# Kernel optimization log

Measured on AMD Instinct MI355X. Metric: run time of the kernel, lower is better.

The kernel has to match this reference:

```python
import jax, jax.numpy as jnp
import numpy as np

NUM_NODES = 100000
NUM_EDGES = 400000
EPS = 1e-9


def _find(parent, u):
    # chase parent pointers to the root (no path compression; parent is
    # immutable within one find, so this terminates because union-by-rank
    # keeps the forest acyclic)
    return jax.lax.while_loop(lambda v: parent[v] != v, lambda v: parent[v], u)


def _kruskal(scores, edge_index, num_nodes):
    """Greedy Kruskal over edges sorted by descending score, via union-find.
    Returns b in {0,1}^E with exactly (num_nodes-1) ones if the graph is
    connected (fewer otherwise), identical acceptance set to the torch loop."""
    E = scores.shape[0]
    order = jnp.argsort(-scores)  # descending
    src = edge_index[0].astype(jnp.int32)
    dst = edge_index[1].astype(jnp.int32)
    max_used = jnp.int32(num_nodes - 1)

    def step(carry, idx):
        parent, rank, b, used = carry
        i = src[idx]
        j = dst[idx]
        ru = _find(parent, i)
        rv = _find(parent, j)
        accept = (ru != rv) & (used < max_used)
        ri = rank[ru]
        rj = rank[rv]
        # union by rank: if ri<rj attach ru under rv, else attach rv under ru;
        # if ranks equal, root ru gains rank (matches the torch union())
        child = jnp.where(ri < rj, ru, rv)
        root = jnp.where(ri < rj, rv, ru)
        parent = parent.at[child].set(jnp.where(accept, root, parent[child]))
        rank = rank.at[root].add(jnp.where(accept & (ri == rj), jnp.int32(1), jnp.int32(0)))
        b = b.at[idx].set(accept.astype(b.dtype))
        used = used + accept.astype(used.dtype)
        return (parent, rank, b, used), None

    parent0 = jnp.arange(num_nodes, dtype=jnp.int32)
    rank0 = jnp.zeros(num_nodes, dtype=jnp.int32)
    b0 = jnp.zeros(E, dtype=scores.dtype)
    (parent, rank, b, used), _ = jax.lax.scan(step, (parent0, rank0, b0, jnp.int32(0)), order)
    return b


def setup_inputs() -> dict:
    key = jax.random.key(0)
    k1, k2, k3 = jax.random.split(key, 3)
    s = jax.random.normal(k1, (NUM_EDGES,), dtype=jnp.float32)
    u = jax.random.uniform(k2, (NUM_EDGES,), dtype=jnp.float32)
    edge_index = jax.random.randint(k3, (2, NUM_EDGES), 0, NUM_NODES, dtype=jnp.int32)
    return {"s": s, "u": u, "edge_index": edge_index, "num_nodes": NUM_NODES}


def reference(s, u, edge_index, num_nodes):
    s_prob = jax.nn.sigmoid(s)
    gumbel = -jnp.log(-jnp.log(u + EPS) + EPS)
    scores = s_prob + gumbel
    return _kruskal(scores, edge_index, num_nodes)
```

## Files before the change

### kernel.cpp

```cpp
#include <hip/hip_runtime.h>
#include <stdint.h>

#define V_NODES 100000
#define MAX_ROUNDS 13
#define TB 256
#define RPT 4
#define TBL 2048
#define TBL_FROM 3

struct alignas(16) Rec { unsigned long long k; unsigned int a, b; };

__device__ __forceinline__ unsigned long long make_key(float sv, float uv, int id) {
    float sp = 1.0f / (1.0f + expf(-sv));
    float g  = -logf(-logf(uv + 1e-9f) + 1e-9f);
    unsigned int b = __float_as_uint(sp + g);
    unsigned int m = (b & 0x80000000u) ? ~b : (b | 0x80000000u);
    return ((unsigned long long)(~m) << 19) | (unsigned long long)(unsigned)id;
}

__device__ __forceinline__ int find_root(const int* __restrict__ parent, int v) {
    int p = parent[v];
    int pp = parent[p];
    while (p != pp) { p = pp; pp = parent[p]; }
    return p;
}

__device__ __forceinline__ void gbid(unsigned long long* __restrict__ best,
                                     unsigned int* __restrict__ guess,
                                     unsigned int root, unsigned long long k) {
    unsigned int kh = (unsigned int)(k >> 32);
    unsigned int g = guess[root];
    if (kh > g) return;
    if (kh < g) guess[root] = kh;
    atomicMin(&best[root], k);
}

__global__ void k_scan0(const float* __restrict__ s, const float* __restrict__ u,
                        const int* __restrict__ src, const int* __restrict__ dst,
                        float* __restrict__ out, unsigned long long* __restrict__ best,
                        unsigned int* __restrict__ guess,
                        Rec* __restrict__ recs, int* __restrict__ parent,
                        int* __restrict__ flags, int E) {
    int base = (blockIdx.x * TB + threadIdx.x) * RPT;

    float sv[RPT], uv[RPT];
    unsigned int a[RPT], b[RPT];
    #pragma unroll
    for (int j = 0; j < RPT; ++j) {
        int e = base + j;
        if (e < E) { sv[j] = s[e]; uv[j] = u[e]; a[j] = src[e]; b[j] = dst[e]; }
    }

    Rec r[RPT];
    #pragma unroll
    for (int j = 0; j < RPT; ++j) {
        int e = base + j;
        if (e >= E) continue;
        r[j].k = make_key(sv[j], uv[j], e);
        r[j].a = a[j]; r[j].b = b[j];
        recs[e] = r[j];
        out[e] = 0.0f;
        if (e < V_NODES) parent[e] = e;
        if (e < MAX_ROUNDS) flags[e] = (e == 0) ? 1 : 0;
    }

    #pragma unroll
    for (int j = 0; j < RPT; ++j) {
        int e = base + j;
        if (e >= E || a[j] == b[j]) continue;
        gbid(best, guess, a[j], r[j].k);
        gbid(best, guess, b[j], r[j].k);
    }
}

__global__ void k_scan_early(const int* __restrict__ parent,
                             unsigned long long* __restrict__ bestC,
                             unsigned int* __restrict__ guess,
                             Rec* __restrict__ recs, int* __restrict__ flags,
                             int r, int E) {
    __shared__ int sflag;
    if (flags[r - 1] == 0) return;
    if (threadIdx.x == 0) sflag = 0;
    __syncthreads();

    int base = (blockIdx.x * TB + threadIdx.x) * RPT;
    bool cross = false;

    Rec rec[RPT];
    int pa[RPT], pb[RPT];
    bool live[RPT];
    #pragma unroll
    for (int j = 0; j < RPT; ++j) {
        int i = base + j;
        if (i < E) rec[j] = recs[i];
        else { rec[j].a = 0; rec[j].b = 0; }
        live[j] = (rec[j].a != rec[j].b);
    }
    #pragma unroll
    for (int j = 0; j < RPT; ++j)
        if (live[j]) { pa[j] = parent[rec[j].a]; pb[j] = parent[rec[j].b]; }

    #pragma unroll
    for (int j = 0; j < RPT; ++j) {
        if (!live[j]) continue;
        int i = base + j;
        int ra = pa[j], rb = pb[j];
        int p = parent[ra]; while (ra != p) { ra = p; p = parent[ra]; }
        p = parent[rb];     while (rb != p) { rb = p; p = parent[rb]; }
        if (ra == rb) {
            *(uint2*)&recs[i].a = make_uint2((unsigned)ra, (unsigned)ra);
        } else {
            cross = true;
            if ((unsigned)ra != rec[j].a || (unsigned)rb != rec[j].b)
                *(uint2*)&recs[i].a = make_uint2((unsigned)ra, (unsigned)rb);
            gbid(bestC, guess, (unsigned)ra, rec[j].k);
            gbid(bestC, guess, (unsigned)rb, rec[j].k);
        }
    }
    if (cross) sflag = 1;
    __syncthreads();
    if (threadIdx.x == 0 && sflag) flags[r] = 1;
}

__global__ void k_scan_tbl(const int* __restrict__ parent,
                           unsigned long long* __restrict__ bestC,
                           unsigned int* __restrict__ guess,
                           Rec* __restrict__ recs, int* __restrict__ flags,
                           int r, int E) {
    __shared__ int sflag;
    __shared__ unsigned int tag[TBL];
    __shared__ unsigned long long tkey[TBL];
    if (flags[r - 1] == 0) return;
    for (int t = threadIdx.x; t < TBL; t += TB) { tag[t] = 0xFFFFFFFFu; tkey[t] = ~0ULL; }
    if (threadIdx.x == 0) sflag = 0;
    __syncthreads();

    int base = (blockIdx.x * TB + threadIdx.x) * RPT;
    bool cross = false;

    Rec rec[RPT];
    int pa[RPT], pb[RPT];
    bool live[RPT];
    #pragma unroll
    for (int j = 0; j < RPT; ++j) {
        int i = base + j;
        if (i < E) rec[j] = recs[i];
        else { rec[j].a = 0; rec[j].b = 0; }
        live[j] = (rec[j].a != rec[j].b);
    }
    #pragma unroll
    for (int j = 0; j < RPT; ++j)
        if (live[j]) { pa[j] = parent[rec[j].a]; pb[j] = parent[rec[j].b]; }
    #pragma unroll
    for (int j = 0; j < RPT; ++j)
        if (live[j]) { pa[j] = parent[pa[j]]; pb[j] = parent[pb[j]]; }

    auto bid = [&](unsigned int root, unsigned long long k) {
        unsigned int s1 = root & (TBL - 1);
        unsigned int prev = atomicCAS(&tag[s1], 0xFFFFFFFFu, root);
        if (prev == 0xFFFFFFFFu || prev == root) {
            atomicMin(&tkey[s1], k);
            return;
        }
        unsigned int s2 = (root * 2654435761u >> 19) & (TBL - 1);
        prev = atomicCAS(&tag[s2], 0xFFFFFFFFu, root);
        if (prev == 0xFFFFFFFFu || prev == root) {
            atomicMin(&tkey[s2], k);
            return;
        }
        gbid(bestC, guess, root, k);
    };

    #pragma unroll
    for (int j = 0; j < RPT; ++j) {
        if (!live[j]) continue;
        int i = base + j;
        int ra = pa[j], rb = pb[j];
        int p = parent[ra]; while (ra != p) { ra = p; p = parent[ra]; }
        p = parent[rb];     while (rb != p) { rb = p; p = parent[rb]; }
        if (ra == rb) {
            *(uint2*)&recs[i].a = make_uint2((unsigned)ra, (unsigned)ra);
        } else {
            cross = true;
            if ((unsigned)ra != rec[j].a || (unsigned)rb != rec[j].b)
                *(uint2*)&recs[i].a = make_uint2((unsigned)ra, (unsigned)rb);
            bid((unsigned)ra, rec[j].k);
            bid((unsigned)rb, rec[j].k);
        }
    }
    if (cross) sflag = 1;
    __syncthreads();

    for (int t = threadIdx.x; t < TBL; t += TB) {
        unsigned int rt = tag[t];
        if (rt != 0xFFFFFFFFu) gbid(bestC, guess, rt, tkey[t]);
    }
    if (threadIdx.x == 0 && sflag) flags[r] = 1;
}

__global__ void k_choose(const int* __restrict__ src, const int* __restrict__ dst,
                         int* __restrict__ parent,
                         const unsigned long long* __restrict__ bestC,
                         float* __restrict__ out, const int* __restrict__ flags,
                         int r) {
    if (flags[r] == 0) return;
    int v = blockIdx.x * blockDim.x + threadIdx.x;
    if (v >= V_NODES) return;
    unsigned long long k = bestC[v];
    if ((unsigned)(k >> 51) != 0u) return;
    int id = (int)(unsigned int)(k & 0x7FFFFu);
    int a0 = src[id], b0 = dst[id];
    int ru = find_root(parent, a0);
    int rv = find_root(parent, b0);
    if (ru != a0) parent[a0] = ru;
    if (rv != b0) parent[b0] = rv;
    int other = (ru == v) ? rv : ru;
    out[id] = 1.0f;
    if ((bestC[other] != k || v > other) && other != v) {
        int po = parent[other];
        parent[v] = (po != other) ? po : other;
    }
}

extern "C" void kernel_launch(void* const* d_in, const int* in_sizes, int n_in,
                              void* d_out, int out_size, void* d_ws, size_t ws_size,
                              hipStream_t stream) {
    const float* s  = (const float*)d_in[0];
    const float* u  = (const float*)d_in[1];
    const int*   ei = (const int*)d_in[2];
    const int E = in_sizes[0];
    const int* src = ei;
    const int* dst = ei + E;
    float* out = (float*)d_out;

    char* ws = (char*)d_ws;
    Rec* recs = (Rec*)ws;
    unsigned long long* bestAll = (unsigned long long*)(recs + E);
    int* parent = (int*)(bestAll + (size_t)MAX_ROUNDS * V_NODES);
    unsigned int* guessAll = (unsigned int*)(parent + V_NODES);
    int* flags  = (int*)(guessAll + (size_t)MAX_ROUNDS * V_NODES);

    const int gE4 = (E + TB * RPT - 1) / (TB * RPT);
    const int gV  = (V_NODES + TB - 1) / TB;

    k_scan0<<<gE4, TB, 0, stream>>>(s, u, src, dst, out, bestAll, guessAll,
                                    recs, parent, flags, E);
    k_choose<<<gV, TB, 0, stream>>>(src, dst, parent, bestAll, out, flags, 0);

    for (int r = 1; r < MAX_ROUNDS; ++r) {
        unsigned long long* best_r = bestAll + (size_t)r * V_NODES;
        unsigned int* guess_r = guessAll + (size_t)r * V_NODES;
        if (r < TBL_FROM)
            k_scan_early<<<gE4, TB, 0, stream>>>(parent, best_r, guess_r,
                                                 recs, flags, r, E);
        else
            k_scan_tbl<<<gE4, TB, 0, stream>>>(parent, best_r, guess_r,
                                               recs, flags, r, E);
        k_choose<<<gV, TB, 0, stream>>>(src, dst, parent, best_r, out, flags, r);
    }
}
```

Measured before the change: 270.3 us.

## Replace parent-array union-find with pointer jumping over previous round's best-edge keys

Removes the per-round k_choose kernel and the parent array. Each scan now finds a component root by following the previous round's min-edge hooks, resolving mutual pairs by the lower id. All chosen edges are marked in one final k_mark pass over every round's best arrays. This cuts 13 launches and the parent writes, but root lookup now chases chains of 64-bit best keys plus record loads, which can be long in later rounds.

```diff
diff --git a/kernel.cpp b/kernel.cpp
--- a/kernel.cpp
+++ b/kernel.cpp
@@ -16,13 +16,6 @@
     unsigned int b = __float_as_uint(sp + g);
     unsigned int m = (b & 0x80000000u) ? ~b : (b | 0x80000000u);
     return ((unsigned long long)(~m) << 19) | (unsigned long long)(unsigned)id;
-}
-
-__device__ __forceinline__ int find_root(const int* __restrict__ parent, int v) {
-    int p = parent[v];
-    int pp = parent[p];
-    while (p != pp) { p = pp; pp = parent[p]; }
-    return p;
 }
 
 __device__ __forceinline__ void gbid(unsigned long long* __restrict__ best,
@@ -35,12 +28,27 @@
     atomicMin(&best[root], k);
 }
 
+__device__ __forceinline__ unsigned int resolve(
+        const unsigned long long* __restrict__ bestP,
+        const Rec* __restrict__ recs,
+        unsigned int x, unsigned long long kb) {
+    while (!(kb >> 51)) {
+        unsigned int id = (unsigned int)(kb & 0x7FFFFu);
+        uint2 ab = *(const uint2*)&recs[id].a;
+        unsigned int other = (ab.x == x) ? ab.y : ab.x;
+        if (other == x) break;
+        unsigned long long ko = bestP[other];
+        if (ko == kb && x < other) break;
+        x = other; kb = ko;
+    }
+    return x;
+}
+
 __global__ void k_scan0(const float* __restrict__ s, const float* __restrict__ u,
                         const int* __restrict__ src, const int* __restrict__ dst,
                         float* __restrict__ out, unsigned long long* __restrict__ best,
                         unsigned int* __restrict__ guess,
-                        Rec* __restrict__ recs, int* __restrict__ parent,
-                        int* __restrict__ flags, int E) {
+                        Rec* __restrict__ recs, int* __restrict__ flags, int E) {
     int base = (blockIdx.x * TB + threadIdx.x) * RPT;
 
     float sv[RPT], uv[RPT];
@@ -60,7 +68,6 @@
         r[j].a = a[j]; r[j].b = b[j];
         recs[e] = r[j];
         out[e] = 0.0f;
-        if (e < V_NODES) parent[e] = e;
         if (e < MAX_ROUNDS) flags[e] = (e == 0) ? 1 : 0;
     }
 
@@ -73,7 +80,7 @@
     }
 }
 
-__global__ void k_scan_early(const int* __restrict__ parent,
+__global__ void k_scan_early(const unsigned long long* __restrict__ bestP,
                              unsigned long long* __restrict__ bestC,
                              unsigned int* __restrict__ guess,
                              Rec* __restrict__ recs, int* __restrict__ flags,
@@ -87,7 +94,7 @@
     bool cross = false;
 
     Rec rec[RPT];
-    int pa[RPT], pb[RPT];
+    unsigned long long ka[RPT], kb[RPT];
     bool live[RPT];
     #pragma unroll
     for (int j = 0; j < RPT; ++j) {
@@ -98,23 +105,22 @@
     }
     #pragma unroll
     for (int j = 0; j < RPT; ++j)
-        if (live[j]) { pa[j] = parent[rec[j].a]; pb[j] = parent[rec[j].b]; }
+        if (live[j]) { ka[j] = bestP[rec[j].a]; kb[j] = bestP[rec[j].b]; }
 
     #pragma unroll
     for (int j = 0; j < RPT; ++j) {
         if (!live[j]) continue;
         int i = base + j;
-        int ra = pa[j], rb = pb[j];
-        int p = parent[ra]; while (ra != p) { ra = p; p = parent[ra]; }
-        p = parent[rb];     while (rb != p) { rb = p; p = parent[rb]; }
+        unsigned int ra = resolve(bestP, recs, rec[j].a, ka[j]);
+        unsigned int rb = resolve(bestP, recs, rec[j].b, kb[j]);
         if (ra == rb) {
-            *(uint2*)&recs[i].a = make_uint2((unsigned)ra, (unsigned)ra);
+            *(uint2*)&recs[i].a = make_uint2(ra, ra);
         } else {
             cross = true;
-            if ((unsigned)ra != rec[j].a || (unsigned)rb != rec[j].b)
-                *(uint2*)&recs[i].a = make_uint2((unsigned)ra, (unsigned)rb);
-            gbid(bestC, guess, (unsigned)ra, rec[j].k);
-            gbid(bestC, guess, (unsigned)rb, rec[j].k);
+            if (ra != rec[j].a || rb != rec[j].b)
+                *(uint2*)&recs[i].a = make_uint2(ra, rb);
+            gbid(bestC, guess, ra, rec[j].k);
+            gbid(bestC, guess, rb, rec[j].k);
         }
     }
     if (cross) sflag = 1;
@@ -122,7 +128,7 @@
     if (threadIdx.x == 0 && sflag) flags[r] = 1;
 }
 
-__global__ void k_scan_tbl(const int* __restrict__ parent,
+__global__ void k_scan_tbl(const unsigned long long* __restrict__ bestP,
                            unsigned long long* __restrict__ bestC,
                            unsigned int* __restrict__ guess,
                            Rec* __restrict__ recs, int* __restrict__ flags,
@@ -139,7 +145,7 @@
     bool cross = false;
 
     Rec rec[RPT];
-    int pa[RPT], pb[RPT];
+    unsigned long long ka[RPT], kb[RPT];
     bool live[RPT];
     #pragma unroll
     for (int j = 0; j < RPT; ++j) {
@@ -150,10 +156,7 @@
     }
     #pragma unroll
     for (int j = 0; j < RPT; ++j)
-        if (live[j]) { pa[j] = parent[rec[j].a]; pb[j] = parent[rec[j].b]; }
-    #pragma unroll
-    for (int j = 0; j < RPT; ++j)
-        if (live[j]) { pa[j] = parent[pa[j]]; pb[j] = parent[pb[j]]; }
+        if (live[j]) { ka[j] = bestP[rec[j].a]; kb[j] = bestP[rec[j].b]; }
 
     auto bid = [&](unsigned int root, unsigned long long k) {
         unsigned int s1 = root & (TBL - 1);
@@ -175,17 +178,16 @@
     for (int j = 0; j < RPT; ++j) {
         if (!live[j]) continue;
         int i = base + j;
-        int ra = pa[j], rb = pb[j];
-        int p = parent[ra]; while (ra != p) { ra = p; p = parent[ra]; }
-        p = parent[rb];     while (rb != p) { rb = p; p = parent[rb]; }
+        unsigned int ra = resolve(bestP, recs, rec[j].a, ka[j]);
+        unsigned int rb = resolve(bestP, recs, rec[j].b, kb[j]);
         if (ra == rb) {
-            *(uint2*)&recs[i].a = make_uint2((unsigned)ra, (unsigned)ra);
+            *(uint2*)&recs[i].a = make_uint2(ra, ra);
         } else {
             cross = true;
-            if ((unsigned)ra != rec[j].a || (unsigned)rb != rec[j].b)
-                *(uint2*)&recs[i].a = make_uint2((unsigned)ra, (unsigned)rb);
-            bid((unsigned)ra, rec[j].k);
-            bid((unsigned)rb, rec[j].k);
+            if (ra != rec[j].a || rb != rec[j].b)
+                *(uint2*)&recs[i].a = make_uint2(ra, rb);
+            bid(ra, rec[j].k);
+            bid(rb, rec[j].k);
         }
     }
     if (cross) sflag = 1;
@@ -198,27 +200,14 @@
     if (threadIdx.x == 0 && sflag) flags[r] = 1;
 }
 
-__global__ void k_choose(const int* __restrict__ src, const int* __restrict__ dst,
-                         int* __restrict__ parent,
-                         const unsigned long long* __restrict__ bestC,
-                         float* __restrict__ out, const int* __restrict__ flags,
-                         int r) {
-    if (flags[r] == 0) return;
-    int v = blockIdx.x * blockDim.x + threadIdx.x;
+__global__ void k_mark(const unsigned long long* __restrict__ bestAll,
+                       float* __restrict__ out) {
+    int v = blockIdx.x * TB + threadIdx.x;
     if (v >= V_NODES) return;
-    unsigned long long k = bestC[v];
-    if ((unsigned)(k >> 51) != 0u) return;
-    int id = (int)(unsigned int)(k & 0x7FFFFu);
-    int a0 = src[id], b0 = dst[id];
-    int ru = find_root(parent, a0);
-    int rv = find_root(parent, b0);
-    if (ru != a0) parent[a0] = ru;
-    if (rv != b0) parent[b0] = rv;
-    int other = (ru == v) ? rv : ru;
-    out[id] = 1.0f;
-    if ((bestC[other] != k || v > other) && other != v) {
-        int po = parent[other];
-        parent[v] = (po != other) ? po : other;
+    #pragma unroll
+    for (int r = 0; r < MAX_ROUNDS; ++r) {
+        unsigned long long k = bestAll[(size_t)r * V_NODES + v];
+        if (!(k >> 51)) out[(unsigned int)(k & 0x7FFFFu)] = 1.0f;
     }
 }
 
@@ -236,26 +225,26 @@
     char* ws = (char*)d_ws;
     Rec* recs = (Rec*)ws;
     unsigned long long* bestAll = (unsigned long long*)(recs + E);
-    int* parent = (int*)(bestAll + (size_t)MAX_ROUNDS * V_NODES);
-    unsigned int* guessAll = (unsigned int*)(parent + V_NODES);
+    unsigned int* guessAll = (unsigned int*)(bestAll + (size_t)MAX_ROUNDS * V_NODES);
     int* flags  = (int*)(guessAll + (size_t)MAX_ROUNDS * V_NODES);
 
     const int gE4 = (E + TB * RPT - 1) / (TB * RPT);
     const int gV  = (V_NODES + TB - 1) / TB;
 
     k_scan0<<<gE4, TB, 0, stream>>>(s, u, src, dst, out, bestAll, guessAll,
-                                    recs, parent, flags, E);
-    k_choose<<<gV, TB, 0, stream>>>(src, dst, parent, bestAll, out, flags, 0);
+                                    recs, flags, E);
 
     for (int r = 1; r < MAX_ROUNDS; ++r) {
+        unsigned long long* best_p = bestAll + (size_t)(r - 1) * V_NODES;
         unsigned long long* best_r = bestAll + (size_t)r * V_NODES;
         unsigned int* guess_r = guessAll + (size_t)r * V_NODES;
         if (r < TBL_FROM)
-            k_scan_early<<<gE4, TB, 0, stream>>>(parent, best_r, guess_r,
+            k_scan_early<<<gE4, TB, 0, stream>>>(best_p, best_r, guess_r,
                                                  recs, flags, r, E);
         else
-            k_scan_tbl<<<gE4, TB, 0, stream>>>(parent, best_r, guess_r,
+            k_scan_tbl<<<gE4, TB, 0, stream>>>(best_p, best_r, guess_r,
                                                recs, flags, r, E);
-        k_choose<<<gV, TB, 0, stream>>>(src, dst, parent, best_r, out, flags, r);
-    }
-}
+    }
+
+    k_mark<<<gV, TB, 0, stream>>>(bestAll, out);
+}
```

Measured after the change: 304.2 us. +12.5%, slower.
